# Kernel optimization log

Hardware: AMD Instinct MI355X
Metric: run time of the kernel (lower is better)

## Reference

```python
import jax, jax.numpy as jnp
import numpy as np

EPS = 1e-08


def setup_inputs() -> dict:
    key = jax.random.key(0)
    k1, k2 = jax.random.split(key)
    N, D, C = 8192, 512, 1000
    features = jax.random.uniform(k1, (N, D), dtype=jnp.float32)
    logits = jax.random.normal(k2, (N, C), dtype=jnp.float32)
    return {"features": features, "logits": logits}


def reference(features, logits):
    N = features.shape[0]
    # softmax over classes, plus eps (matches F.softmax(...) + eps)
    p = jax.nn.softmax(logits, axis=1) + EPS                     # [N, C]
    # similarity matrix with diagonal removed
    cos_sim = features @ features.T - jnp.eye(N, dtype=features.dtype)  # [N, N]
    neighbor_mask = (cos_sim >= -1).astype(cos_sim.dtype)
    w = cos_sim * neighbor_mask
    w = w / jnp.sum(w, axis=1, keepdims=True)                    # row-normalized weights
    weighted_sum_nb = w @ p                                      # [N, C]
    # F.kl_div(log_input, target, reduction='batchmean')
    # = sum(target * (log(target) - log_input)) / N
    kl = jnp.sum(weighted_sum_nb * (jnp.log(weighted_sum_nb) - jnp.log(p))) / N
    return kl
```

## Files before the change

kernel.cpp:

```cpp
#include <hip/hip_runtime.h>
#include <math.h>

#define NN 8192
#define DD 512
#define CC 1000
#define CP 1024
#define CPD (CP*DD)

typedef __attribute__((ext_vector_type(8))) short short8;
typedef __attribute__((ext_vector_type(4))) float f32x4;
typedef __attribute__((ext_vector_type(4))) unsigned short us4;
typedef __attribute__((ext_vector_type(8))) unsigned short us8;
typedef __attribute__((ext_vector_type(4))) unsigned int ui4;

__device__ __forceinline__ float bf2f(unsigned short u){
  union{unsigned int i; float f;} v; v.i = ((unsigned int)u)<<16; return v.f;
}
__device__ __forceinline__ unsigned short f2bf(float f){
  union{float f; unsigned int i;} v; v.f = f;
  unsigned int r = v.i + 0x7FFF + ((v.i>>16)&1);
  return (unsigned short)(r>>16);
}
__device__ __forceinline__ float waveRedSum(float v){
  #pragma unroll
  for(int o=32;o;o>>=1) v += __shfl_xor(v,o,64);
  return v;
}
__device__ __forceinline__ float waveRedMax(float v){
  #pragma unroll
  for(int o=32;o;o>>=1) v = fmaxf(v,__shfl_xor(v,o,64));
  return v;
}
__device__ __forceinline__ void gload_lds16(const void* g, void* l){
  __builtin_amdgcn_global_load_lds((const __attribute__((address_space(1))) void*)g,
                                   (__attribute__((address_space(3))) void*)l, 16, 0, 0);
}

__global__ __launch_bounds__(256) void k_prep(const float* __restrict__ F,
                                              const float* __restrict__ L,
                                              unsigned short* __restrict__ FbT,
                                              unsigned short* __restrict__ Fb,
                                              float* __restrict__ gpart,
                                              unsigned short* __restrict__ PbT){
  __shared__ __align__(16) char smem[8*1028*4];
  int bid = blockIdx.x;
  int grp = bid/3, r = bid - grp*3;
  int t = threadIdx.x;

  if(r < 2){
    int cb = grp*2 + r;
    unsigned short* lds = (unsigned short*)smem;
    float* gq = (float*)(smem + 64*68*2);
    int i0 = (cb & 127)*64, d0 = (cb >> 7)*64;
    int cx = t&15, ry = t>>4;
    float ca0=0.f,ca1=0.f,ca2=0.f,ca3=0.f;
    #pragma unroll
    for(int rr=0;rr<4;rr++){
      int row = rr*16 + ry;
      f32x4 fv = *(const f32x4*)&F[(size_t)(i0+row)*DD + d0 + cx*4];
      us4 u; u[0]=f2bf(fv[0]); u[1]=f2bf(fv[1]); u[2]=f2bf(fv[2]); u[3]=f2bf(fv[3]);
      *(us4*)&lds[row*68 + cx*4] = u;
      *(us4*)&Fb[(size_t)(i0+row)*DD + d0 + cx*4] = u;
      ca0+=fv[0]; ca1+=fv[1]; ca2+=fv[2]; ca3+=fv[3];
    }
    {
      f32x4 cv; cv[0]=ca0; cv[1]=ca1; cv[2]=ca2; cv[3]=ca3;
      *(f32x4*)&gq[ry*64 + cx*4] = cv;
    }
    __syncthreads();
    #pragma unroll
    for(int rr=0;rr<4;rr++){
      int d = rr*16 + ry;
      us4 u;
      #pragma unroll
      for(int q=0;q<4;q++) u[q] = lds[(cx*4+q)*68 + d];
      *(us4*)&FbT[(size_t)(d0+d)*NN + i0 + cx*4] = u;
    }
    __syncthreads();
    if(t<64){
      float s=0.f;
      #pragma unroll
      for(int j=0;j<16;j++) s += gq[j*64+t];
      gpart[(cb&127)*DD + d0 + t] = s;
    }
  } else {
    int sb = grp;
    unsigned int (*lt)[1028] = (unsigned int(*)[1028])smem;
    int l = t&63, w = t>>6;
    int i0 = sb*16;
    #pragma unroll
    for(int q=0;q<4;q++){
      int rr = w*4 + q;
      int row = i0 + rr;
      const float* lr = L + (size_t)row*CC;
      float v[16]; float mx = -1e30f;
      #pragma unroll
      for(int k=0;k<16;k++){ int c = l + 64*k; v[k] = (c<CC)? lr[c] : -1e30f; mx = fmaxf(mx,v[k]); }
      mx = waveRedMax(mx);
      float s = 0.f;
      #pragma unroll
      for(int k=0;k<16;k++){ v[k] = __expf(v[k]-mx); s += v[k]; }
      s = waveRedSum(s);
      float inv = 1.0f/s;
      #pragma unroll
      for(int k=0;k<16;k++){
        int c = l + 64*k;
        float p = v[k]*inv + 1e-8f;
        unsigned short h = (c<CC)? f2bf(p) : (unsigned short)0;
        *((unsigned short*)&lt[rr>>1][c] + (rr&1)) = h;
      }
    }
    __syncthreads();
    #pragma unroll
    for(int k=0;k<4;k++){
      int c = t + 256*k;
      ui4 a, b;
      #pragma unroll
      for(int j=0;j<4;j++){ a[j] = lt[j][c]; b[j] = lt[j+4][c]; }
      *(ui4*)&PbT[(size_t)c*NN + i0]     = a;
      *(ui4*)&PbT[(size_t)c*NN + i0 + 8] = b;
    }
  }
}

__global__ __launch_bounds__(256,2) void k_gemm1(const unsigned short* __restrict__ A,
                                                 const unsigned short* __restrict__ B,
                                                 unsigned short* __restrict__ Tpb,
                                                 const float* __restrict__ gpart,
                                                 float* __restrict__ g){
  __shared__ __align__(16) unsigned short smem[4*8192];
  __shared__ float rs[4][64];
  int bid = blockIdx.x;
  int t = threadIdx.x;
  if(bid < 8){
    int d = bid*64 + (t&63);
    int q = t>>6;
    float s = 0.f;
    #pragma unroll
    for(int j=0;j<32;j++) s += gpart[(size_t)(q*32+j)*DD + d];
    rs[q][t&63] = s;
    __syncthreads();
    if(q==0) g[d] = rs[0][t&63]+rs[1][t&63]+rs[2][t&63]+rs[3][t&63];
    return;
  }
  int gb = bid - 8;
  int Lsw = (gb&7)*64 + (gb>>3);
  int l = t&63, w = t>>6;
  int bx = Lsw & 7, by = (Lsw>>3) & 3, bz = Lsw>>5;
  int m0 = bx*128, n0 = by*128;
  int k0 = bz*512;
  int wm = w>>1, wn = w&1;
  f32x4 acc[4][4] = {};
  int srow = w*32 + (l>>3);
  int scl  = (l&7) ^ (srow&7);
  const unsigned short* Ab = A + (size_t)(m0 + srow)*NN + k0 + scl*8;
  const unsigned short* Bb = B + (size_t)(n0 + srow)*NN + k0 + scl*8;
  int ldsOff = (w*32)*64;

  #pragma unroll
  for(int q=0;q<4;q++){
    gload_lds16(Ab + (size_t)q*8*NN, smem + ldsOff + q*8*64);
    gload_lds16(Bb + (size_t)q*8*NN, smem + 8192 + ldsOff + q*8*64);
  }
  int cur = 0;
  for(int kt=0; kt<512; kt+=64){
    if(kt+64 < 512){
      unsigned short* An = smem + (cur^1)*16384 + ldsOff;
      unsigned short* Bn = smem + (cur^1)*16384 + 8192 + ldsOff;
      #pragma unroll
      for(int q=0;q<4;q++){
        gload_lds16(Ab + (size_t)q*8*NN + kt + 64, An + q*8*64);
        gload_lds16(Bb + (size_t)q*8*NN + kt + 64, Bn + q*8*64);
      }
      asm volatile("s_waitcnt vmcnt(8)" ::: "memory");
    } else {
      asm volatile("s_waitcnt vmcnt(0)" ::: "memory");
    }
    __builtin_amdgcn_s_barrier();
    const unsigned short* Ac = smem + cur*16384;
    const unsigned short* Bc = smem + cur*16384 + 8192;
    #pragma unroll
    for(int ks=0;ks<2;ks++){
      short8 af[4], bf[4];
      #pragma unroll
      for(int mi=0;mi<4;mi++){
        int rr = wm*64 + mi*16 + (l&15);
        int ch = ((ks<<2) + (l>>4)) ^ (rr&7);
        af[mi] = *(const short8*)&Ac[rr*64 + ch*8];
      }
      #pragma unroll
      for(int ni=0;ni<4;ni++){
        int rr = wn*64 + ni*16 + (l&15);
        int ch = ((ks<<2) + (l>>4)) ^ (rr&7);
        bf[ni] = *(const short8*)&Bc[rr*64 + ch*8];
      }
      #pragma unroll
      for(int mi=0;mi<4;mi++)
        #pragma unroll
        for(int ni=0;ni<4;ni++)
          acc[mi][ni] = __builtin_amdgcn_mfma_f32_16x16x32_bf16(af[mi], bf[ni], acc[mi][ni], 0,0,0);
    }
    __builtin_amdgcn_s_barrier();
    cur ^= 1;
  }
  unsigned short* Tz = Tpb + (size_t)bz*CPD;
  int rbase = (l>>4)*4;
  #pragma unroll
  for(int mi=0;mi<4;mi++){
    int c = m0 + wm*64 + mi*16 + rbase;
    #pragma unroll
    for(int ni=0;ni<4;ni++){
      int d = n0 + wn*64 + ni*16 + (l&15);
      #pragma unroll
      for(int j=0;j<4;j++)
        Tz[(size_t)(c+j)*DD + d] = f2bf(acc[mi][ni][j]);
    }
  }
}

__global__ __launch_bounds__(256) void k_redT(const unsigned short* __restrict__ Tpb,
                                              const unsigned short* __restrict__ Fb,
                                              const float* __restrict__ g,
                                              unsigned short* __restrict__ Ttb,
                                              float* __restrict__ invr){
  int t = threadIdx.x;
  size_t i = ((size_t)blockIdx.x*256 + (size_t)t)*8;
  f32x4 s0 = {0.f,0.f,0.f,0.f}, s1 = {0.f,0.f,0.f,0.f};
  #pragma unroll
  for(int z=0;z<16;z++){
    us8 v = *(const us8*)&Tpb[(size_t)z*CPD + i];
    s0[0]+=bf2f(v[0]); s0[1]+=bf2f(v[1]); s0[2]+=bf2f(v[2]); s0[3]+=bf2f(v[3]);
    s1[0]+=bf2f(v[4]); s1[1]+=bf2f(v[5]); s1[2]+=bf2f(v[6]); s1[3]+=bf2f(v[7]);
  }
  us8 u;
  u[0]=f2bf(s0[0]); u[1]=f2bf(s0[1]); u[2]=f2bf(s0[2]); u[3]=f2bf(s0[3]);
  u[4]=f2bf(s1[0]); u[5]=f2bf(s1[1]); u[6]=f2bf(s1[2]); u[7]=f2bf(s1[3]);
  *(us8*)&Ttb[i] = u;
  int row = blockIdx.x*32 + (t>>3);
  int seg = (t&7)*64;
  const unsigned short* fr = Fb + (size_t)row*DD + seg;
  const float* gr = g + seg;
  float s = 0.f;
  #pragma unroll
  for(int j=0;j<8;j++){
    us8 f8 = *(const us8*)&fr[j*8];
    f32x4 ga = *(const f32x4*)&gr[j*8];
    f32x4 gb = *(const f32x4*)&gr[j*8+4];
    s += bf2f(f8[0])*ga[0]+bf2f(f8[1])*ga[1]+bf2f(f8[2])*ga[2]+bf2f(f8[3])*ga[3]
       + bf2f(f8[4])*gb[0]+bf2f(f8[5])*gb[1]+bf2f(f8[6])*gb[2]+bf2f(f8[7])*gb[3];
  }
  s += __shfl_xor(s,1,64); s += __shfl_xor(s,2,64); s += __shfl_xor(s,4,64);
  if((t&7)==0) invr[row] = 1.0f/(s - 1.0f);
}

__global__ __launch_bounds__(256,2) void k_gemm2(const unsigned short* __restrict__ Fb,
                                                 const unsigned short* __restrict__ Bt,
                                                 const unsigned short* __restrict__ PbT,
                                                 const float* __restrict__ invr,
                                                 float* __restrict__ partials){
  __shared__ __align__(16) unsigned short smem[4*8192];
  __shared__ float red[4];
  int bid = blockIdx.x;
  int Lsw = (bid&7)*64 + (bid>>3);
  int t = threadIdx.x, l = t&63, w = t>>6;
  int m0 = (Lsw>>3)*128, n0 = (Lsw&7)*128;
  int wm = w>>1, wn = w&1;
  f32x4 acc[4][4] = {};
  int srow = w*32 + (l>>3);
  int scl  = (l&7) ^ (srow&7);
  const unsigned short* Ab = Fb + (size_t)(m0 + srow)*DD + scl*8;
  const unsigned short* Bb = Bt + (size_t)(n0 + srow)*DD + scl*8;
  int ldsOff = (w*32)*64;

  #pragma unroll
  for(int q=0;q<4;q++){
    gload_lds16(Ab + (size_t)q*8*DD, smem + ldsOff + q*8*64);
    gload_lds16(Bb + (size_t)q*8*DD, smem + 8192 + ldsOff + q*8*64);
  }
  int cur = 0;
  for(int kt=0; kt<512; kt+=64){
    if(kt+64 < 512){
      unsigned short* An = smem + (cur^1)*16384 + ldsOff;
      unsigned short* Bn = smem + (cur^1)*16384 + 8192 + ldsOff;
      #pragma unroll
      for(int q=0;q<4;q++){
        gload_lds16(Ab + (size_t)q*8*DD + kt + 64, An + q*8*64);
        gload_lds16(Bb + (size_t)q*8*DD + kt + 64, Bn + q*8*64);
      }
      asm volatile("s_waitcnt vmcnt(8)" ::: "memory");
    } else {
      asm volatile("s_waitcnt vmcnt(0)" ::: "memory");
    }
    __builtin_amdgcn_s_barrier();
    const unsigned short* Ac = smem + cur*16384;
    const unsigned short* Bc = smem + cur*16384 + 8192;
    #pragma unroll
    for(int ks=0;ks<2;ks++){
      short8 af[4], bf[4];
      #pragma unroll
      for(int mi=0;mi<4;mi++){
        int rr = wm*64 + mi*16 + (l&15);
        int ch = ((ks<<2) + (l>>4)) ^ (rr&7);
        af[mi] = *(const short8*)&Ac[rr*64 + ch*8];
      }
      #pragma unroll
      for(int ni=0;ni<4;ni++){
        int rr = wn*64 + ni*16 + (l&15);
        int ch = ((ks<<2) + (l>>4)) ^ (rr&7);
        bf[ni] = *(const short8*)&Bc[rr*64 + ch*8];
      }
      #pragma unroll
      for(int mi=0;mi<4;mi++)
        #pragma unroll
        for(int ni=0;ni<4;ni++)
          acc[mi][ni] = __builtin_amdgcn_mfma_f32_16x16x32_bf16(af[mi], bf[ni], acc[mi][ni], 0,0,0);
    }
    __builtin_amdgcn_s_barrier();
    cur ^= 1;
  }
  __syncthreads();
  #pragma unroll
  for(int j=0;j<8;j++){
    int e = j*256 + t;
    int row = e >> 4;
    int ch  = e & 15;
    us8 v = *(const us8*)&PbT[(size_t)(n0+row)*NN + m0 + ch*8];
    *(us8*)&smem[row*136 + ch*8] = v;
  }
  __syncthreads();
  float kl = 0.f;
  int rbase = (l>>4)*4;
  #pragma unroll
  for(int mi=0;mi<4;mi++){
    int i_base = m0 + wm*64 + mi*16 + rbase;
    int ci = wm*64 + mi*16 + rbase;
    f32x4 ir4 = *(const f32x4*)&invr[i_base];
    #pragma unroll
    for(int ni=0;ni<4;ni++){
      int cr = wn*64 + ni*16 + (l&15);
      int c = n0 + cr;
      if(c < CC){
        us4 p4 = *(const us4*)&smem[cr*136 + ci];
        #pragma unroll
        for(int j=0;j<4;j++){
          float p = bf2f(p4[j]);
          float ws = (acc[mi][ni][j] - p) * ir4[j];
          kl += ws * (__logf(ws) - __logf(p));
        }
      }
    }
  }
  kl = waveRedSum(kl);
  if(l==0) red[w]=kl;
  __syncthreads();
  if(t==0) partials[Lsw] = red[0]+red[1]+red[2]+red[3];
}

__global__ __launch_bounds__(64) void k_finalize(const float* __restrict__ partials,
                                                 float* __restrict__ out){
  int l = threadIdx.x;
  double s = 0.0;
  for(int j=l; j<512; j+=64) s += (double)partials[j];
  #pragma unroll
  for(int o=32;o;o>>=1) s += __shfl_xor(s,o,64);
  if(l==0) out[0] = (float)(s / (double)NN);
}

extern "C" void kernel_launch(void* const* d_in, const int* in_sizes, int n_in,
                              void* d_out, int out_size, void* d_ws, size_t ws_size,
                              hipStream_t stream){
  const float* F = (const float*)d_in[0];
  const float* L = (const float*)d_in[1];
  float* out = (float*)d_out;

  unsigned char* w8 = (unsigned char*)d_ws;
  unsigned short* FbT = (unsigned short*)w8;
  unsigned short* PbT = (unsigned short*)(w8 + (8u<<20));
  unsigned short* Tpb = (unsigned short*)(w8 + (24u<<20));
  unsigned short* Ttb = (unsigned short*)(w8 + (40u<<20));
  unsigned short* Fb  = (unsigned short*)(w8 + (41u<<20));
  float* gpart        = (float*)(w8 + (49u<<20));
  float* g            = (float*)(w8 + (49u<<20) + 262144);
  float* invr         = (float*)(w8 + (49u<<20) + 264192);
  float* partials     = (float*)(w8 + (49u<<20) + 296960);

  hipLaunchKernelGGL(k_prep,     dim3(1536),   dim3(256), 0, stream, F, L, FbT, Fb, gpart, PbT);
  hipLaunchKernelGGL(k_gemm1,    dim3(520),    dim3(256), 0, stream, PbT, FbT, Tpb, gpart, g);
  hipLaunchKernelGGL(k_redT,     dim3(256),    dim3(256), 0, stream, Tpb, Fb, g, Ttb, invr);
  hipLaunchKernelGGL(k_gemm2,    dim3(512),    dim3(256), 0, stream, Fb, Ttb, PbT, invr, partials);
  hipLaunchKernelGGL(k_finalize, dim3(1),      dim3(64),  0, stream, partials, out);
}
```

Baseline: 66.55 us.

## Halve gemm1 split-K count, vectorize softmax loads, fuse finalize via atomicAdd

The first GEMM's split-K factor drops from 16 to 8, so each block covers K=1024. That halves the partial buffer the reduction kernel sums, but gemm1 now launches 256 work blocks instead of 512. The softmax prep branch now reads logits as float4 and transposes through a 16-row bf16 LDS tile, storing 8-element vectors. The finalize kernel is removed: gemm2 blocks atomically add their scaled partial KL into the output, which k_prep zeroes. This saves a launch but makes the float summation order nondeterministic.

```diff
diff --git a/kernel.cpp b/kernel.cpp
--- a/kernel.cpp
+++ b/kernel.cpp
@@ -11,7 +11,6 @@
 typedef __attribute__((ext_vector_type(4))) float f32x4;
 typedef __attribute__((ext_vector_type(4))) unsigned short us4;
 typedef __attribute__((ext_vector_type(8))) unsigned short us8;
-typedef __attribute__((ext_vector_type(4))) unsigned int ui4;
 
 __device__ __forceinline__ float bf2f(unsigned short u){
   union{unsigned int i; float f;} v; v.i = ((unsigned int)u)<<16; return v.f;
@@ -41,11 +40,13 @@
                                               unsigned short* __restrict__ FbT,
                                               unsigned short* __restrict__ Fb,
                                               float* __restrict__ gpart,
-                                              unsigned short* __restrict__ PbT){
-  __shared__ __align__(16) char smem[8*1028*4];
+                                              unsigned short* __restrict__ PbT,
+                                              float* __restrict__ out){
+  __shared__ __align__(16) char smem[16*1032*2];
   int bid = blockIdx.x;
   int grp = bid/3, r = bid - grp*3;
   int t = threadIdx.x;
+  if(bid==0 && t==0) out[0] = 0.f;
 
   if(r < 2){
     int cb = grp*2 + r;
@@ -85,7 +86,7 @@
     }
   } else {
     int sb = grp;
-    unsigned int (*lt)[1028] = (unsigned int(*)[1028])smem;
+    unsigned short (*lt)[1032] = (unsigned short(*)[1032])smem;
     int l = t&63, w = t>>6;
     int i0 = sb*16;
     #pragma unroll
@@ -95,30 +96,41 @@
       const float* lr = L + (size_t)row*CC;
       float v[16]; float mx = -1e30f;
       #pragma unroll
-      for(int k=0;k<16;k++){ int c = l + 64*k; v[k] = (c<CC)? lr[c] : -1e30f; mx = fmaxf(mx,v[k]); }
+      for(int k=0;k<4;k++){
+        int c4 = l*4 + 256*k;
+        f32x4 fv;
+        if(c4 < CC) fv = *(const f32x4*)&lr[c4];
+        else { fv[0]=-1e30f; fv[1]=-1e30f; fv[2]=-1e30f; fv[3]=-1e30f; }
+        v[4*k+0]=fv[0]; v[4*k+1]=fv[1]; v[4*k+2]=fv[2]; v[4*k+3]=fv[3];
+        mx = fmaxf(mx, fmaxf(fmaxf(fv[0],fv[1]), fmaxf(fv[2],fv[3])));
+      }
       mx = waveRedMax(mx);
       float s = 0.f;
       #pragma unroll
-      for(int k=0;k<16;k++){ v[k] = __expf(v[k]-mx); s += v[k]; }
+      for(int e=0;e<16;e++){ v[e] = __expf(v[e]-mx); s += v[e]; }
       s = waveRedSum(s);
       float inv = 1.0f/s;
       #pragma unroll
-      for(int k=0;k<16;k++){
-        int c = l + 64*k;
-        float p = v[k]*inv + 1e-8f;
-        unsigned short h = (c<CC)? f2bf(p) : (unsigned short)0;
-        *((unsigned short*)&lt[rr>>1][c] + (rr&1)) = h;
+      for(int k=0;k<4;k++){
+        int c4 = l*4 + 256*k;
+        us4 u;
+        #pragma unroll
+        for(int j=0;j<4;j++){
+          float p = v[4*k+j]*inv + 1e-8f;
+          u[j] = (c4+j < CC)? f2bf(p) : (unsigned short)0;
+        }
+        *(us4*)&lt[rr][c4] = u;
       }
     }
     __syncthreads();
     #pragma unroll
     for(int k=0;k<4;k++){
       int c = t + 256*k;
-      ui4 a, b;
-      #pragma unroll
-      for(int j=0;j<4;j++){ a[j] = lt[j][c]; b[j] = lt[j+4][c]; }
-      *(ui4*)&PbT[(size_t)c*NN + i0]     = a;
-      *(ui4*)&PbT[(size_t)c*NN + i0 + 8] = b;
+      us8 a, b;
+      #pragma unroll
+      for(int j=0;j<8;j++){ a[j] = lt[j][c]; b[j] = lt[j+8][c]; }
+      *(us8*)&PbT[(size_t)c*NN + i0]     = a;
+      *(us8*)&PbT[(size_t)c*NN + i0 + 8] = b;
     }
   }
 }
@@ -144,11 +156,11 @@
     return;
   }
   int gb = bid - 8;
-  int Lsw = (gb&7)*64 + (gb>>3);
+  int Lsw = (gb&7)*32 + (gb>>3);
   int l = t&63, w = t>>6;
   int bx = Lsw & 7, by = (Lsw>>3) & 3, bz = Lsw>>5;
   int m0 = bx*128, n0 = by*128;
-  int k0 = bz*512;
+  int k0 = bz*1024;
   int wm = w>>1, wn = w&1;
   f32x4 acc[4][4] = {};
   int srow = w*32 + (l>>3);
@@ -163,8 +175,8 @@
     gload_lds16(Bb + (size_t)q*8*NN, smem + 8192 + ldsOff + q*8*64);
   }
   int cur = 0;
-  for(int kt=0; kt<512; kt+=64){
-    if(kt+64 < 512){
+  for(int kt=0; kt<1024; kt+=64){
+    if(kt+64 < 1024){
       unsigned short* An = smem + (cur^1)*16384 + ldsOff;
       unsigned short* Bn = smem + (cur^1)*16384 + 8192 + ldsOff;
       #pragma unroll
@@ -227,7 +239,7 @@
   size_t i = ((size_t)blockIdx.x*256 + (size_t)t)*8;
   f32x4 s0 = {0.f,0.f,0.f,0.f}, s1 = {0.f,0.f,0.f,0.f};
   #pragma unroll
-  for(int z=0;z<16;z++){
+  for(int z=0;z<8;z++){
     us8 v = *(const us8*)&Tpb[(size_t)z*CPD + i];
     s0[0]+=bf2f(v[0]); s0[1]+=bf2f(v[1]); s0[2]+=bf2f(v[2]); s0[3]+=bf2f(v[3]);
     s1[0]+=bf2f(v[4]); s1[1]+=bf2f(v[5]); s1[2]+=bf2f(v[6]); s1[3]+=bf2f(v[7]);
@@ -257,7 +269,7 @@
                                                  const unsigned short* __restrict__ Bt,
                                                  const unsigned short* __restrict__ PbT,
                                                  const float* __restrict__ invr,
-                                                 float* __restrict__ partials){
+                                                 float* __restrict__ out){
   __shared__ __align__(16) unsigned short smem[4*8192];
   __shared__ float red[4];
   int bid = blockIdx.x;
@@ -353,17 +365,7 @@
   kl = waveRedSum(kl);
   if(l==0) red[w]=kl;
   __syncthreads();
-  if(t==0) partials[Lsw] = red[0]+red[1]+red[2]+red[3];
-}
-
-__global__ __launch_bounds__(64) void k_finalize(const float* __restrict__ partials,
-                                                 float* __restrict__ out){
-  int l = threadIdx.x;
-  double s = 0.0;
-  for(int j=l; j<512; j+=64) s += (double)partials[j];
-  #pragma unroll
-  for(int o=32;o;o>>=1) s += __shfl_xor(s,o,64);
-  if(l==0) out[0] = (float)(s / (double)NN);
+  if(t==0) atomicAdd(out, (red[0]+red[1]+red[2]+red[3]) * (1.0f/(float)NN));
 }
 
 extern "C" void kernel_launch(void* const* d_in, const int* in_sizes, int n_in,
@@ -377,16 +379,14 @@
   unsigned short* FbT = (unsigned short*)w8;
   unsigned short* PbT = (unsigned short*)(w8 + (8u<<20));
   unsigned short* Tpb = (unsigned short*)(w8 + (24u<<20));
-  unsigned short* Ttb = (unsigned short*)(w8 + (40u<<20));
-  unsigned short* Fb  = (unsigned short*)(w8 + (41u<<20));
-  float* gpart        = (float*)(w8 + (49u<<20));
-  float* g            = (float*)(w8 + (49u<<20) + 262144);
-  float* invr         = (float*)(w8 + (49u<<20) + 264192);
-  float* partials     = (float*)(w8 + (49u<<20) + 296960);
-
-  hipLaunchKernelGGL(k_prep,     dim3(1536),   dim3(256), 0, stream, F, L, FbT, Fb, gpart, PbT);
-  hipLaunchKernelGGL(k_gemm1,    dim3(520),    dim3(256), 0, stream, PbT, FbT, Tpb, gpart, g);
-  hipLaunchKernelGGL(k_redT,     dim3(256),    dim3(256), 0, stream, Tpb, Fb, g, Ttb, invr);
-  hipLaunchKernelGGL(k_gemm2,    dim3(512),    dim3(256), 0, stream, Fb, Ttb, PbT, invr, partials);
-  hipLaunchKernelGGL(k_finalize, dim3(1),      dim3(64),  0, stream, partials, out);
-}
+  unsigned short* Ttb = (unsigned short*)(w8 + (32u<<20));
+  unsigned short* Fb  = (unsigned short*)(w8 + (33u<<20));
+  float* gpart        = (float*)(w8 + (41u<<20));
+  float* g            = (float*)(w8 + (41u<<20) + 262144);
+  float* invr         = (float*)(w8 + (41u<<20) + 264192);
+
+  hipLaunchKernelGGL(k_prep,  dim3(1536), dim3(256), 0, stream, F, L, FbT, Fb, gpart, PbT, out);
+  hipLaunchKernelGGL(k_gemm1, dim3(264),  dim3(256), 0, stream, PbT, FbT, Tpb, gpart, g);
+  hipLaunchKernelGGL(k_redT,  dim3(256),  dim3(256), 0, stream, Tpb, Fb, g, Ttb, invr);
+  hipLaunchKernelGGL(k_gemm2, dim3(512),  dim3(256), 0, stream, Fb, Ttb, PbT, invr, out);
+}
```

New measurement: 70.69 us. 1.06x slower.
